# Kernel optimization log

Measured on AMD Instinct MI355X. Metric: run time of the kernel, lower is better.

## Reference

```python
import jax, jax.numpy as jnp
import numpy as np

# Dimensions matching init_kwargs
B, S, D, d_feat, O = 64, 1024, 64, 2, 10
L = S // 2  # label_site
STD = 0.01  # 'random_eye' init noise scale


def setup_inputs() -> dict:
    key = jax.random.key(0)
    k1, k2, k3, k4 = jax.random.split(key, 4)
    x = jax.random.normal(k1, (B, S, d_feat), dtype=jnp.float32)
    # InputRegion tensors, bond_str 'slri': eye over (l, r) broadcast over (s, i)
    W_left = jnp.eye(D, dtype=jnp.float32)[None, :, :, None] \
        + STD * jax.random.normal(k2, (L, D, D, d_feat), dtype=jnp.float32)
    W_right = jnp.eye(D, dtype=jnp.float32)[None, :, :, None] \
        + STD * jax.random.normal(k3, (S - L, D, D, d_feat), dtype=jnp.float32)
    # OutputSite tensor, bond_str 'olr': eye over (l, r) broadcast over o
    out_core = jnp.eye(D, dtype=jnp.float32)[None, :, :] \
        + STD * jax.random.normal(k4, (O, D, D), dtype=jnp.float32)
    return {"x": x, "W_left": W_left, "out_core": out_core, "W_right": W_right}


def reference(x, W_left, out_core, W_right):
    # x: [B, S, d]; W_left: [L, D, D, d]; out_core: [O, D, D]; W_right: [S-L, D, D, d]
    Ls = W_left.shape[0]
    Dv = W_left.shape[1]
    Bv = x.shape[0]
    # Per-site matrices (einsum 'slri,bsi->bslr'), laid out scan-major [S, B, D, D]
    mats_l = jnp.einsum('slri,bsi->sblr', W_left, x[:, :Ls])
    mats_r = jnp.einsum('slri,bsi->sblr', W_right, x[:, Ls:])
    # Open boundary edge vectors e = [1, 0, ..., 0]
    e = jnp.zeros((Dv,), dtype=x.dtype).at[0].set(1.0)
    v0 = jnp.broadcast_to(e, (Bv, Dv))
    # Left-to-right vector propagation through left chain
    def lstep(v, m):
        return jnp.einsum('bl,blr->br', v, m), None
    vL, _ = jax.lax.scan(lstep, v0, mats_l)
    # Right-to-left vector propagation through right chain
    def rstep(w, m):
        return jnp.einsum('blr,br->bl', m, w), None
    wR, _ = jax.lax.scan(rstep, v0, mats_r, reverse=True)
    # Contract through the output core: [B, O]
    return jnp.einsum('bl,olr,br->bo', vL, out_core, wR)
```

## Files before the change

kernel.cpp:

```cpp
#include <hip/hip_runtime.h>
#include <stdint.h>

#define NSITE 512
#define DD    64
#define NB    64
#define NO    10
#define NSEG  16
#define SEGLEN 32
#define SLAB_BYTES 32768
#define PACK_BYTES 16384

typedef short bf16x8 __attribute__((ext_vector_type(8)));
typedef float f32x16 __attribute__((ext_vector_type(16)));

__device__ __forceinline__ uint32_t pk2(float a, float b) {
    return __builtin_amdgcn_perm(__float_as_uint(b), __float_as_uint(a), 0x07060302);
}

__global__ __launch_bounds__(256) void pack_kernel(float* __restrict__ wl,
                                                   float* __restrict__ wr) {
    const int g = blockIdx.x;
    const int right = (g >= NSITE) ? 1 : 0;
    const int s = right ? g - NSITE : g;
    float* base = (right ? wr : wl) + (size_t)s * (SLAB_BYTES / 4);

    __shared__ float2 st[DD * 65];
    const float2* src2 = (const float2*)base;
    for (int e = threadIdx.x; e < DD * DD; e += 256)
        st[(e >> 6) * 65 + (e & 63)] = src2[e];
    __syncthreads();

    uint32_t* out = (uint32_t*)base;
    #pragma unroll
    for (int rr = 0; rr < 16; ++rr) {
        const int od = rr * 256 + threadIdx.x;
        const int chunk = od >> 8, i = chunk >> 3, sk = chunk & 7;
        const int H = (od >> 7) & 1, m5 = (od >> 2) & 31, d = od & 3;
        const int m = 32 * i + m5, k = 8 * sk + 4 * H + d;
        const float2 a = right ? st[m * 65 + k] : st[k * 65 + m];
        out[od] = pk2(a.x, a.y);
    }
}

__device__ __forceinline__ void dma16(const void* gp, void* lp) {
    __builtin_amdgcn_global_load_lds(
        (const __attribute__((address_space(1))) uint32_t*)gp,
        (__attribute__((address_space(3))) uint32_t*)lp, 16, 0, 0);
}

__global__ __launch_bounds__(256, 2) void stage1_kernel(
        const float* __restrict__ x, float* __restrict__ wl, float* __restrict__ wr) {
    const int bid  = blockIdx.x;
    const int side = bid >> 8;
    const int seg  = (bid >> 4) & 15;
    const int bq   = bid & 15;
    const int wave = threadIdx.x >> 6;
    const int lane = threadIdx.x & 63;
    const int b    = bq * 4 + wave;
    const int m5   = lane & 31;
    const int H    = lane >> 5;

    __shared__ __align__(16) char ring[4][PACK_BYTES];
    __shared__ float2 xs[4][SEGLEN];

    char* wbuf = (char*)(side ? wr : wl);

    if (lane < SEGLEN) {
        const float2* xp = ((const float2*)x) + (size_t)b * 1024 + (side ? NSITE : 0);
        const int sg = seg * SEGLEN + (side ? SEGLEN - 1 - lane : lane);
        xs[wave][lane] = xp[sg];
    }

    auto siteAddr = [&](int t) -> const char* {
        const int sg = seg * SEGLEN + (side ? SEGLEN - 1 - t : t);
        return wbuf + (size_t)sg * SLAB_BYTES;
    };

    #pragma unroll
    for (int t0 = 0; t0 < 2; ++t0) {
        const char* sb = siteAddr(t0);
        #pragma unroll
        for (int c = 0; c < 4; ++c) {
            const int ch = wave * 4 + c;
            dma16(sb + ch * 1024 + lane * 16, ring[t0] + ch * 1024);
        }
    }

    f32x16 acc[2][2];
    #pragma unroll
    for (int i = 0; i < 2; ++i)
        #pragma unroll
        for (int j = 0; j < 2; ++j)
            #pragma unroll
            for (int q = 0; q < 16; ++q) {
                const int row = (q & 3) + 8 * (q >> 2) + 4 * H;
                acc[i][j][q] = (i == j && row == m5) ? 1.f : 0.f;
            }

    for (int t = 0; t < SEGLEN; ++t) {
        int t2 = t + 2; if (t2 > SEGLEN - 1) t2 = SEGLEN - 1;
        {
            const char* sb = siteAddr(t2);
            char* lb = ring[(t + 2) & 3];
            #pragma unroll
            for (int c = 0; c < 4; ++c) {
                const int ch = wave * 4 + c;
                dma16(sb + ch * 1024 + lane * 16, lb + ch * 1024);
            }
        }
        asm volatile("s_waitcnt vmcnt(8)" ::: "memory");
        asm volatile("s_barrier" ::: "memory");

        const char* rb = ring[t & 3];
        uint4 af[2][8];
        #pragma unroll
        for (int i = 0; i < 2; ++i)
            #pragma unroll
            for (int sk = 0; sk < 8; ++sk)
                af[i][sk] = *(const uint4*)(rb + (i * 8 + sk) * 1024 + lane * 16);

        const float2 xv = xs[wave][t];
        f32x16 nacc[2][2] = {};
        #pragma unroll
        for (int sk = 0; sk < 8; ++sk) {
            const int mi = sk >> 2, qb = 4 * (sk & 3);
            union { bf16x8 v; uint32_t u[4]; } bf[2];
            #pragma unroll
            for (int j = 0; j < 2; ++j)
                #pragma unroll
                for (int dlt = 0; dlt < 4; ++dlt) {
                    const float v = acc[mi][j][qb + dlt];
                    bf[j].u[dlt] = pk2(xv.x * v, xv.y * v);
                }
            #pragma unroll
            for (int i = 0; i < 2; ++i) {
                union { bf16x8 v; uint4 u; } a; a.u = af[i][sk];
                #pragma unroll
                for (int j = 0; j < 2; ++j)
                    nacc[i][j] = __builtin_amdgcn_mfma_f32_32x32x16_bf16(
                        a.v, bf[j].v, nacc[i][j], 0, 0, 0);
            }
        }
        #pragma unroll
        for (int i = 0; i < 2; ++i)
            #pragma unroll
            for (int j = 0; j < 2; ++j)
                acc[i][j] = nacc[i][j];
    }

    {
        const int p = b * NSEG + seg;
        char* pdst = wbuf + (size_t)(p >> 1) * SLAB_BYTES + PACK_BYTES + (p & 1) * 8192;
        #pragma unroll
        for (int i = 0; i < 2; ++i)
            #pragma unroll
            for (int j = 0; j < 2; ++j) {
                const int c = 32 * j + m5;
                #pragma unroll
                for (int Q = 0; Q < 4; ++Q) {
                    const int r0 = 32 * i + 8 * Q + 4 * H;
                    uint2 val;
                    val.x = pk2(acc[i][j][4 * Q + 0], acc[i][j][4 * Q + 1]);
                    val.y = pk2(acc[i][j][4 * Q + 2], acc[i][j][4 * Q + 3]);
                    *(uint2*)(pdst + c * 128 + r0 * 2) = val;
                }
            }
    }
    asm volatile("s_waitcnt vmcnt(0)" ::: "memory");
}

__global__ __launch_bounds__(256) void stage2_kernel(
        const float* __restrict__ wl, const float* __restrict__ wr,
        float* __restrict__ vbuf) {
    const int chain = blockIdx.x;
    const int side  = chain >> 6, b = chain & 63;
    const int tid   = threadIdx.x, r = tid & 63, cg = tid >> 6;
    const char* wbuf = (const char*)(side ? wr : wl);

    __shared__ float vsh[DD];
    __shared__ float part[4][DD];
    if (tid < DD) vsh[tid] = (tid == 0) ? 1.f : 0.f;
    __syncthreads();

    for (int gi = 0; gi < NSEG; ++gi) {
        const int g = side ? (NSEG - 1 - gi) : gi;
        const int p = b * NSEG + g;
        const uint16_t* P = (const uint16_t*)(wbuf
            + (size_t)(p >> 1) * SLAB_BYTES + PACK_BYTES + (p & 1) * 8192);
        float acc = 0.f;
        #pragma unroll
        for (int cc = 0; cc < 16; ++cc) {
            const int c = cg * 16 + cc;
            const float pv = __uint_as_float(((uint32_t)P[c * 64 + r]) << 16);
            acc = fmaf(vsh[c], pv, acc);
        }
        part[cg][r] = acc;
        __syncthreads();
        if (tid < DD) vsh[tid] = part[0][tid] + part[1][tid] + part[2][tid] + part[3][tid];
        __syncthreads();
    }
    if (tid < DD) vbuf[chain * DD + tid] = vsh[tid];
}

__global__ __launch_bounds__(64) void finalize_kernel(
        const float* __restrict__ core,
        const float* __restrict__ vbuf,
        float* __restrict__ out) {
    const int b    = blockIdx.x;
    const int lane = threadIdx.x;
    __shared__ float vls[DD];
    vls[lane] = vbuf[b * DD + lane];
    const float wr = vbuf[(NB + b) * DD + lane];
    __syncthreads();
    for (int o = 0; o < NO; ++o) {
        float acc = 0.f;
        #pragma unroll 8
        for (int l = 0; l < DD; ++l)
            acc += vls[l] * core[(o * DD + l) * DD + lane];
        acc *= wr;
        #pragma unroll
        for (int off = 32; off > 0; off >>= 1)
            acc += __shfl_xor(acc, off, 64);
        if (lane == 0) out[b * NO + o] = acc;
    }
}

extern "C" void kernel_launch(void* const* d_in, const int* in_sizes, int n_in,
                              void* d_out, int out_size, void* d_ws, size_t ws_size,
                              hipStream_t stream) {
    const float* x    = (const float*)d_in[0];
    float*       wl   = (float*)d_in[1];
    const float* core = (const float*)d_in[2];
    float*       wr   = (float*)d_in[3];
    float* vbuf = (float*)d_ws;

    pack_kernel<<<2 * NSITE, 256, 0, stream>>>(wl, wr);
    stage1_kernel<<<512, 256, 0, stream>>>(x, wl, wr);
    stage2_kernel<<<2 * NB, 256, 0, stream>>>(wl, wr, vbuf);
    finalize_kernel<<<NB, DD, 0, stream>>>(core, vbuf, (float*)d_out);
}
```

Before: 182.1 us.

## Deepen stage1 prefetch, ping-pong accumulators, packed muls, fuse stage2 with finalize

In stage1 the prefetch ring depth rises from two sites ahead to three, with the vmcnt wait adjusted to match. The per-step accumulator copy is replaced by ping-ponging two accumulator sets through a lambda body. The x-scaling now uses v_pk_mul_f32 inline asm. The separate stage2 and finalize kernels are merged into one tail kernel per batch that runs both chains and the output contraction, removing one launch and the workspace round trip. The trade-off is that the tail runs only 64 blocks, each serializing two chains over 16 segments.

```diff
diff --git a/kernel.cpp b/kernel.cpp
--- a/kernel.cpp
+++ b/kernel.cpp
@@ -77,7 +77,7 @@
     };
 
     #pragma unroll
-    for (int t0 = 0; t0 < 2; ++t0) {
+    for (int t0 = 0; t0 < 3; ++t0) {
         const char* sb = siteAddr(t0);
         #pragma unroll
         for (int c = 0; c < 4; ++c) {
@@ -86,7 +86,7 @@
         }
     }
 
-    f32x16 acc[2][2];
+    f32x16 accP[2][2], accQ[2][2];
     #pragma unroll
     for (int i = 0; i < 2; ++i)
         #pragma unroll
@@ -94,21 +94,21 @@
             #pragma unroll
             for (int q = 0; q < 16; ++q) {
                 const int row = (q & 3) + 8 * (q >> 2) + 4 * H;
-                acc[i][j][q] = (i == j && row == m5) ? 1.f : 0.f;
-            }
-
-    for (int t = 0; t < SEGLEN; ++t) {
-        int t2 = t + 2; if (t2 > SEGLEN - 1) t2 = SEGLEN - 1;
+                accP[i][j][q] = (i == j && row == m5) ? 1.f : 0.f;
+            }
+
+    auto body = [&](int t, f32x16 (&tin)[2][2], f32x16 (&tout)[2][2]) {
+        int t3 = t + 3; if (t3 > SEGLEN - 1) t3 = SEGLEN - 1;
         {
-            const char* sb = siteAddr(t2);
-            char* lb = ring[(t + 2) & 3];
+            const char* sb = siteAddr(t3);
+            char* lb = ring[(t + 3) & 3];
             #pragma unroll
             for (int c = 0; c < 4; ++c) {
                 const int ch = wave * 4 + c;
                 dma16(sb + ch * 1024 + lane * 16, lb + ch * 1024);
             }
         }
-        asm volatile("s_waitcnt vmcnt(8)" ::: "memory");
+        asm volatile("s_waitcnt vmcnt(12)" ::: "memory");
         asm volatile("s_barrier" ::: "memory");
 
         const char* rb = ring[t & 3];
@@ -120,32 +120,48 @@
                 af[i][sk] = *(const uint4*)(rb + (i * 8 + sk) * 1024 + lane * 16);
 
         const float2 xv = xs[wave][t];
-        f32x16 nacc[2][2] = {};
+        float2 x01; x01.x = xv.x; x01.y = xv.y;
+
+        #pragma unroll
+        for (int i = 0; i < 2; ++i)
+            #pragma unroll
+            for (int j = 0; j < 2; ++j)
+                tout[i][j] = 0;
+
         #pragma unroll
         for (int sk = 0; sk < 8; ++sk) {
             const int mi = sk >> 2, qb = 4 * (sk & 3);
             union { bf16x8 v; uint32_t u[4]; } bf[2];
             #pragma unroll
-            for (int j = 0; j < 2; ++j)
+            for (int j = 0; j < 2; ++j) {
                 #pragma unroll
-                for (int dlt = 0; dlt < 4; ++dlt) {
-                    const float v = acc[mi][j][qb + dlt];
-                    bf[j].u[dlt] = pk2(xv.x * v, xv.y * v);
+                for (int e = 0; e < 2; ++e) {
+                    float2 vp;
+                    vp.x = tin[mi][j][qb + 2 * e];
+                    vp.y = tin[mi][j][qb + 2 * e + 1];
+                    float2 d0, d1;
+                    asm("v_pk_mul_f32 %0, %1, %2 op_sel:[0,0] op_sel_hi:[1,0]"
+                        : "=v"(d0) : "v"(x01), "v"(vp));
+                    asm("v_pk_mul_f32 %0, %1, %2 op_sel:[0,1] op_sel_hi:[1,1]"
+                        : "=v"(d1) : "v"(x01), "v"(vp));
+                    bf[j].u[2 * e]     = pk2(d0.x, d0.y);
+                    bf[j].u[2 * e + 1] = pk2(d1.x, d1.y);
                 }
+            }
             #pragma unroll
             for (int i = 0; i < 2; ++i) {
                 union { bf16x8 v; uint4 u; } a; a.u = af[i][sk];
                 #pragma unroll
                 for (int j = 0; j < 2; ++j)
-                    nacc[i][j] = __builtin_amdgcn_mfma_f32_32x32x16_bf16(
-                        a.v, bf[j].v, nacc[i][j], 0, 0, 0);
-            }
-        }
-        #pragma unroll
-        for (int i = 0; i < 2; ++i)
-            #pragma unroll
-            for (int j = 0; j < 2; ++j)
-                acc[i][j] = nacc[i][j];
+                    tout[i][j] = __builtin_amdgcn_mfma_f32_32x32x16_bf16(
+                        a.v, bf[j].v, tout[i][j], 0, 0, 0);
+            }
+        }
+    };
+
+    for (int t = 0; t < SEGLEN; t += 2) {
+        body(t,     accP, accQ);
+        body(t + 1, accQ, accP);
     }
 
     {
@@ -160,8 +176,8 @@
                 for (int Q = 0; Q < 4; ++Q) {
                     const int r0 = 32 * i + 8 * Q + 4 * H;
                     uint2 val;
-                    val.x = pk2(acc[i][j][4 * Q + 0], acc[i][j][4 * Q + 1]);
-                    val.y = pk2(acc[i][j][4 * Q + 2], acc[i][j][4 * Q + 3]);
+                    val.x = pk2(accP[i][j][4 * Q + 0], accP[i][j][4 * Q + 1]);
+                    val.y = pk2(accP[i][j][4 * Q + 2], accP[i][j][4 * Q + 3]);
                     *(uint2*)(pdst + c * 128 + r0 * 2) = val;
                 }
             }
@@ -169,59 +185,51 @@
     asm volatile("s_waitcnt vmcnt(0)" ::: "memory");
 }
 
-__global__ __launch_bounds__(256) void stage2_kernel(
+__global__ __launch_bounds__(256) void tail_kernel(
         const float* __restrict__ wl, const float* __restrict__ wr,
-        float* __restrict__ vbuf) {
-    const int chain = blockIdx.x;
-    const int side  = chain >> 6, b = chain & 63;
-    const int tid   = threadIdx.x, r = tid & 63, cg = tid >> 6;
-    const char* wbuf = (const char*)(side ? wr : wl);
-
-    __shared__ float vsh[DD];
-    __shared__ float part[4][DD];
-    if (tid < DD) vsh[tid] = (tid == 0) ? 1.f : 0.f;
+        const float* __restrict__ core, float* __restrict__ out) {
+    const int b    = blockIdx.x;
+    const int tid  = threadIdx.x;
+    const int side = tid >> 7;
+    const int half = (tid >> 6) & 1;
+    const int r    = tid & 63;
+
+    __shared__ float vs[2][DD];
+    __shared__ float part[2][2][DD];
+    if (half == 0) vs[side][r] = (r == 0) ? 1.f : 0.f;
     __syncthreads();
 
+    const char* wb = (const char*)(side ? wr : wl);
     for (int gi = 0; gi < NSEG; ++gi) {
         const int g = side ? (NSEG - 1 - gi) : gi;
         const int p = b * NSEG + g;
-        const uint16_t* P = (const uint16_t*)(wbuf
+        const uint16_t* P = (const uint16_t*)(wb
             + (size_t)(p >> 1) * SLAB_BYTES + PACK_BYTES + (p & 1) * 8192);
         float acc = 0.f;
         #pragma unroll
-        for (int cc = 0; cc < 16; ++cc) {
-            const int c = cg * 16 + cc;
-            const float pv = __uint_as_float(((uint32_t)P[c * 64 + r]) << 16);
-            acc = fmaf(vsh[c], pv, acc);
-        }
-        part[cg][r] = acc;
+        for (int cc = 0; cc < 32; ++cc) {
+            const int c = half * 32 + cc;
+            acc = fmaf(vs[side][c],
+                       __uint_as_float(((uint32_t)P[c * 64 + r]) << 16), acc);
+        }
+        part[side][half][r] = acc;
         __syncthreads();
-        if (tid < DD) vsh[tid] = part[0][tid] + part[1][tid] + part[2][tid] + part[3][tid];
+        if (half == 0) vs[side][r] = part[side][0][r] + part[side][1][r];
         __syncthreads();
     }
-    if (tid < DD) vbuf[chain * DD + tid] = vsh[tid];
-}
-
-__global__ __launch_bounds__(64) void finalize_kernel(
-        const float* __restrict__ core,
-        const float* __restrict__ vbuf,
-        float* __restrict__ out) {
-    const int b    = blockIdx.x;
-    const int lane = threadIdx.x;
-    __shared__ float vls[DD];
-    vls[lane] = vbuf[b * DD + lane];
-    const float wr = vbuf[(NB + b) * DD + lane];
-    __syncthreads();
-    for (int o = 0; o < NO; ++o) {
-        float acc = 0.f;
+
+    const int og   = tid >> 6;
+    const int lane = tid & 63;
+    for (int o = og; o < NO; o += 4) {
+        float a = 0.f;
         #pragma unroll 8
         for (int l = 0; l < DD; ++l)
-            acc += vls[l] * core[(o * DD + l) * DD + lane];
-        acc *= wr;
+            a += vs[0][l] * core[(o * DD + l) * DD + lane];
+        a *= vs[1][lane];
         #pragma unroll
         for (int off = 32; off > 0; off >>= 1)
-            acc += __shfl_xor(acc, off, 64);
-        if (lane == 0) out[b * NO + o] = acc;
+            a += __shfl_xor(a, off, 64);
+        if (lane == 0) out[b * NO + o] = a;
     }
 }
 
@@ -232,10 +240,8 @@
     float*       wl   = (float*)d_in[1];
     const float* core = (const float*)d_in[2];
     float*       wr   = (float*)d_in[3];
-    float* vbuf = (float*)d_ws;
 
     pack_kernel<<<2 * NSITE, 256, 0, stream>>>(wl, wr);
     stage1_kernel<<<512, 256, 0, stream>>>(x, wl, wr);
-    stage2_kernel<<<2 * NB, 256, 0, stream>>>(wl, wr, vbuf);
-    finalize_kernel<<<NB, DD, 0, stream>>>(core, vbuf, (float*)d_out);
-}
+    tail_kernel<<<NB, 256, 0, stream>>>(wl, wr, core, (float*)d_out);
+}
```

After: 198.1 us. 8.8% more time.
